# Optimization experiments

Measured on AMD Instinct MI355X. Metric: run time of the kernel, lower is better.

## Reference

```python
import jax, jax.numpy as jnp
import numpy as np

HEADS = 12
EPS = 1e-5

def setup_inputs() -> dict:
    key = jax.random.key(0)
    ks = jax.random.split(key, 24)
    B, T, H = 128, 128, 768
    RIN, RH, NT = 512, 512, 10
    s = 0.02
    inp = {
        'slot_vector': jax.random.normal(ks[0], (B, H), jnp.float32),
        'utt_vectors': jax.random.normal(ks[1], (B, T, H), jnp.float32),
        'Wq': jax.random.normal(ks[2], (H, H), jnp.float32) * s,
        'bq': jnp.zeros((H,), jnp.float32),
        'Wk': jax.random.normal(ks[3], (H, H), jnp.float32) * s,
        'bk': jnp.zeros((H,), jnp.float32),
        'Wv': jax.random.normal(ks[4], (H, H), jnp.float32) * s,
        'bv': jnp.zeros((H,), jnp.float32),
        'Wo': jax.random.normal(ks[5], (H, H), jnp.float32) * s,
        'bo': jnp.zeros((H,), jnp.float32),
        'W_in': jax.random.normal(ks[6], (RIN, 2 * H), jnp.float32) * s,
        'b_in': jnp.zeros((RIN,), jnp.float32),
        'W_ih': jax.random.normal(ks[7], (4 * RH, RIN), jnp.float32) * s,
        'W_hh': jax.random.normal(ks[8], (4 * RH, RH), jnp.float32) * s,
        'b_ih': jnp.zeros((4 * RH,), jnp.float32),
        'b_hh': jnp.zeros((4 * RH,), jnp.float32),
        'W_tag': jax.random.normal(ks[9], (NT, RH), jnp.float32) * s,
        'b_tag': jnp.zeros((NT,), jnp.float32),
        'ln_g': jnp.ones((NT,), jnp.float32),
        'ln_b': jnp.zeros((NT,), jnp.float32),
    }
    return inp

def _forward(slot_vector, utt_vectors, Wq, bq, Wk, bk, Wv, bv, Wo, bo,
             W_in, b_in, W_ih, W_hh, b_ih, b_hh, W_tag, b_tag, ln_g, ln_b):
    B, T, H = utt_vectors.shape
    dk = H // HEADS
    # Multi-head attention: Q is slot vector (seq len 1), K/V are utt encodings
    q = (slot_vector @ Wq.T + bq).reshape(B, 1, HEADS, dk).transpose(0, 2, 1, 3)  # [B,h,1,dk]
    k = (utt_vectors @ Wk.T + bk).reshape(B, T, HEADS, dk).transpose(0, 2, 1, 3)  # [B,h,T,dk]
    v = (utt_vectors @ Wv.T + bv).reshape(B, T, HEADS, dk).transpose(0, 2, 1, 3)
    scores = jnp.einsum('bhqd,bhkd->bhqk', q, k) / jnp.sqrt(jnp.float32(dk))
    attn = jax.nn.softmax(scores, axis=-1)
    X = jnp.einsum('bhqk,bhkd->bhqd', attn, v).transpose(0, 2, 1, 3).reshape(B, H)
    X = X @ Wo.T + bo  # [B, H] context vector, fixed across timesteps
    RH = W_hh.shape[1]
    h0 = jnp.zeros((B, RH), jnp.float32)
    c0 = jnp.zeros((B, RH), jnp.float32)

    def step(carry, x_t):
        h, c = carry
        lstm_in = jax.nn.sigmoid(jnp.concatenate([x_t, X], axis=1) @ W_in.T + b_in)
        gates = lstm_in @ W_ih.T + b_ih + h @ W_hh.T + b_hh  # [B, 4*RH]
        i_g, f_g, g_g, o_g = jnp.split(gates, 4, axis=1)  # torch gate order i,f,g,o
        c = jax.nn.sigmoid(f_g) * c + jax.nn.sigmoid(i_g) * jnp.tanh(g_g)
        h = jax.nn.sigmoid(o_g) * jnp.tanh(c)
        y = h @ W_tag.T + b_tag  # [B, NT]
        mu = jnp.mean(y, axis=-1, keepdims=True)
        var = jnp.mean((y - mu) ** 2, axis=-1, keepdims=True)
        y = (y - mu) / jnp.sqrt(var + EPS) * ln_g + ln_b
        return (h, c), y

    xs = utt_vectors.transpose(1, 0, 2)  # [T, B, H]
    _, ys = jax.lax.scan(step, (h0, c0), xs)  # ys: [T, B, NT]
    return ys.transpose(1, 2, 0)  # [B, NT, T]

def reference(slot_vector, utt_vectors, Wq, bq, Wk, bk, Wv, bv, Wo, bo,
              W_in, b_in, W_ih, W_hh, b_ih, b_hh, W_tag, b_tag, ln_g, ln_b):
    return _forward(slot_vector, utt_vectors, Wq, bq, Wk, bk, Wv, bv, Wo, bo,
                    W_in, b_in, W_ih, W_hh, b_ih, b_hh, W_tag, b_tag, ln_g, ln_b)
```

## Files before the change

kernel.cpp:

```cpp
#include <hip/hip_runtime.h>
#include <hip/hip_bf16.h>
#include <math.h>

#define Bc 128
#define Tc 128
#define Hc 768
#define NHEAD 12
#define DKc 64
#define RHc 512
#define G4c 2048
#define NTc 10
#define LNEPS 1e-5f
#define NSLC 8

typedef short bf16x8 __attribute__((ext_vector_type(8)));
typedef float f32x4 __attribute__((ext_vector_type(4)));

__device__ __forceinline__ float sigmoidf_(float x) { return 1.0f / (1.0f + __expf(-x)); }
__device__ __forceinline__ float tanhf_(float x) { return 1.0f - 2.0f / (__expf(2.0f * x) + 1.0f); }

__device__ __forceinline__ ushort f2bf(float f) {
  union { float f; uint u; } c; c.f = f;
  uint r = (c.u + 0x7FFFu + ((c.u >> 16) & 1u)) >> 16;
  return (ushort)r;
}
__device__ __forceinline__ float bf2f(ushort u) {
  union { uint u; float f; } c; c.u = ((uint)u) << 16;
  return c.f;
}
__device__ __forceinline__ uint pack2(float a, float b) {
  return (uint)f2bf(a) | ((uint)f2bf(b) << 16);
}

__global__ void bias_sum_perm_k(const float* __restrict__ a, const float* __restrict__ b,
                                float* __restrict__ o) {
  int i = blockIdx.x * blockDim.x + threadIdx.x;
  if (i < G4c) {
    const int g = i >> 9, u = i & 511;
    o[u * 4 + g] = a[i] + b[i];
  }
}

__global__ void cvt4_k(const float* __restrict__ x, ushort* __restrict__ y, int n4) {
  int i = blockIdx.x * 256 + threadIdx.x;
  if (i < n4) {
    float4 v = ((const float4*)x)[i];
    ushort4 o; o.x = f2bf(v.x); o.y = f2bf(v.y); o.z = f2bf(v.z); o.w = f2bf(v.w);
    ((ushort4*)y)[i] = o;
  }
}

__global__ __launch_bounds__(256) void cvt_wih_perm_k(
    const float* __restrict__ W, ushort* __restrict__ out)
{
  const int rp = blockIdx.x;
  const int u = rp >> 2, g = rp & 3;
  const float* src = W + (size_t)(g * 512 + u) * 512;
  ushort* dst = out + (size_t)rp * 512;
  for (int k = threadIdx.x; k < 512; k += 256) dst[k] = f2bf(src[k]);
}

__global__ __launch_bounds__(256) void cvt_whh_frag_k(
    const float* __restrict__ Whh, ushort* __restrict__ out)
{
  const int idx = blockIdx.x * 256 + threadIdx.x;
  const int lane = idx & 63;
  const int kf = (idx >> 6) & 15;
  const int ti = idx >> 10;
  const int m = lane & 15;
  const int u = (ti >> 3) * 32 + (ti & 7) * 4 + (m >> 2);
  const int gate = m & 3;
  const int k0 = kf * 32 + (lane >> 4) * 8;
  const float* src = Whh + ((size_t)(gate * RHc + u)) * RHc + k0;
  ushort4 o0, o1;
  o0.x = f2bf(src[0]); o0.y = f2bf(src[1]); o0.z = f2bf(src[2]); o0.w = f2bf(src[3]);
  o1.x = f2bf(src[4]); o1.y = f2bf(src[5]); o1.z = f2bf(src[6]); o1.w = f2bf(src[7]);
  ushort* dst = out + (size_t)idx * 8;
  *(ushort4*)dst = o0;
  *(ushort4*)(dst + 4) = o1;
}

__global__ __launch_bounds__(256) void bgemm_bt(
    const void* __restrict__ Aptr, const ushort* __restrict__ Wb,
    const float* __restrict__ bias, void* __restrict__ Cptr,
    int M, int N, int K, int amode, int outMode,
    const float* __restrict__ utt, const float* __restrict__ xo, int trow0)
{
  __shared__ ushort As[128 * 40];
  __shared__ ushort Ws[128 * 40];
  const int tid = threadIdx.x;
  const int lane = tid & 63, wid = tid >> 6;
  const int wm = wid >> 1, wn = wid & 1;
  const int row0 = blockIdx.y * 128, col0 = blockIdx.x * 128;

  f32x4 acc[4][4];
#pragma unroll
  for (int i = 0; i < 4; ++i)
#pragma unroll
    for (int j = 0; j < 4; ++j) {
      f32x4 z = {0.f, 0.f, 0.f, 0.f};
      acc[i][j] = z;
    }

  const int r = tid >> 1, kq = (tid & 1) * 16;

  for (int kb = 0; kb < K; kb += 32) {
    const int k = kb + kq;
    if (amode == 2) {
      const ushort* ap = (const ushort*)Aptr + (size_t)(row0 + r) * K + k;
      *(uint4*)&As[r * 40 + kq] = *(const uint4*)ap;
      *(uint4*)&As[r * 40 + kq + 8] = *(const uint4*)(ap + 8);
    } else {
      const float* ap;
      if (amode == 0) {
        ap = (const float*)Aptr + (size_t)(row0 + r) * K + k;
      } else {
        const int b = r;
        const int t = trow0 + blockIdx.y;
        ap = (k < Hc) ? utt + ((size_t)b * Tc + t) * Hc + k
                      : xo + (size_t)b * Hc + (k - Hc);
      }
      const float4 f0 = *(const float4*)ap;
      const float4 f1 = *(const float4*)(ap + 4);
      const float4 f2 = *(const float4*)(ap + 8);
      const float4 f3 = *(const float4*)(ap + 12);
      uint4 u0, u1;
      u0.x = pack2(f0.x, f0.y); u0.y = pack2(f0.z, f0.w);
      u0.z = pack2(f1.x, f1.y); u0.w = pack2(f1.z, f1.w);
      u1.x = pack2(f2.x, f2.y); u1.y = pack2(f2.z, f2.w);
      u1.z = pack2(f3.x, f3.y); u1.w = pack2(f3.z, f3.w);
      *(uint4*)&As[r * 40 + kq] = u0;
      *(uint4*)&As[r * 40 + kq + 8] = u1;
    }
    {
      const ushort* wp = Wb + (size_t)(col0 + r) * K + k;
      *(uint4*)&Ws[r * 40 + kq] = *(const uint4*)wp;
      *(uint4*)&Ws[r * 40 + kq + 8] = *(const uint4*)(wp + 8);
    }
    __syncthreads();
    const int koff = (lane >> 4) * 8;
    const int ar = wm * 64 + (lane & 15);
    const int wr = wn * 64 + (lane & 15);
    bf16x8 af[4], wf[4];
#pragma unroll
    for (int i = 0; i < 4; ++i) af[i] = *(const bf16x8*)&As[(ar + i * 16) * 40 + koff];
#pragma unroll
    for (int i = 0; i < 4; ++i) wf[i] = *(const bf16x8*)&Ws[(wr + i * 16) * 40 + koff];
#pragma unroll
    for (int fm = 0; fm < 4; ++fm)
#pragma unroll
      for (int fn = 0; fn < 4; ++fn)
        acc[fm][fn] = __builtin_amdgcn_mfma_f32_16x16x32_bf16(af[fm], wf[fn], acc[fm][fn], 0, 0, 0);
    __syncthreads();
  }

#pragma unroll
  for (int fm = 0; fm < 4; ++fm) {
    const int m0 = row0 + wm * 64 + fm * 16 + ((lane >> 4) * 4);
#pragma unroll
    for (int fn = 0; fn < 4; ++fn) {
      const int n = col0 + wn * 64 + fn * 16 + (lane & 15);
      const float bb = bias[n];
#pragma unroll
      for (int q = 0; q < 4; ++q) {
        const float v = acc[fm][fn][q] + bb;
        if (outMode == 1)
          ((ushort*)Cptr)[(size_t)(m0 + q) * N + n] = f2bf(sigmoidf_(v));
        else
          ((float*)Cptr)[(size_t)(m0 + q) * N + n] = v;
      }
    }
  }
}

__global__ __launch_bounds__(256) void fold_qp_k(
    const float* __restrict__ slot, const float* __restrict__ Wq,
    const float* __restrict__ bq, const float* __restrict__ Wk,
    const float* __restrict__ bk, ushort* __restrict__ Pb, float* __restrict__ cqB)
{
  __shared__ float ss[Hc];
  __shared__ float qp[4][DKc];
  __shared__ float qs[DKc];
  const int bx = blockIdx.x;
  const int b = bx / NHEAD, h = bx % NHEAD;
  const int tid = threadIdx.x;
  for (int i = tid; i < Hc; i += 256) ss[i] = slot[(size_t)b * Hc + i];
  __syncthreads();
  {
    const int d = tid & 63, qt = tid >> 6;
    const float* wr = Wq + (size_t)(h * DKc + d) * Hc + qt * 192;
    const float* sb = ss + qt * 192;
    float a = 0.f;
    for (int e = 0; e < 192; e += 4) {
      const float4 wv = *(const float4*)(wr + e);
      a += wv.x * sb[e] + wv.y * sb[e + 1] + wv.z * sb[e + 2] + wv.w * sb[e + 3];
    }
    qp[qt][d] = a;
  }
  __syncthreads();
  if (tid < DKc)
    qs[tid] = qp[0][tid] + qp[1][tid] + qp[2][tid] + qp[3][tid] + bq[h * DKc + tid];
  __syncthreads();
  if (tid < DKc) {
    float pv = qs[tid] * bk[h * DKc + tid];
#pragma unroll
    for (int off = 32; off; off >>= 1) pv += __shfl_xor(pv, off);
    if (tid == 0) cqB[b * NHEAD + h] = pv;
  }
  for (int j = tid; j < Hc; j += 256) {
    float a = 0.f;
#pragma unroll 8
    for (int d = 0; d < DKc; ++d)
      a = fmaf(qs[d], Wk[(size_t)(h * DKc + d) * Hc + j], a);
    Pb[((size_t)b * NHEAD + h) * Hc + j] = f2bf(a);
  }
}

__global__ __launch_bounds__(256) void attn_scores2_k(
    const ushort* __restrict__ Pb, const float* __restrict__ cqB,
    const float* __restrict__ utt, float* __restrict__ Att)
{
  __shared__ float Phs[NHEAD][Hc];
  __shared__ float sc[NHEAD][Tc];
  const int b = blockIdx.x;
  const int tid = threadIdx.x;
  for (int i = tid; i < NHEAD * Hc; i += 256)
    ((float*)Phs)[i] = bf2f(Pb[(size_t)b * NHEAD * Hc + i]);
  __syncthreads();
  const int t = tid & 127, hh = tid >> 7;
  const int h0 = hh * 6;
  float a6[6];
#pragma unroll
  for (int i = 0; i < 6; ++i) a6[i] = 0.f;
  const float* xr = utt + ((size_t)b * Tc + t) * Hc;
  for (int j = 0; j < Hc; j += 4) {
    const float4 xv = *(const float4*)(xr + j);
#pragma unroll
    for (int i = 0; i < 6; ++i) {
      a6[i] = fmaf(xv.x, Phs[h0 + i][j], a6[i]);
      a6[i] = fmaf(xv.y, Phs[h0 + i][j + 1], a6[i]);
      a6[i] = fmaf(xv.z, Phs[h0 + i][j + 2], a6[i]);
      a6[i] = fmaf(xv.w, Phs[h0 + i][j + 3], a6[i]);
    }
  }
#pragma unroll
  for (int i = 0; i < 6; ++i)
    sc[h0 + i][t] = (a6[i] + cqB[b * NHEAD + h0 + i]) * 0.125f;
  __syncthreads();
  const int w = tid >> 6, lane = tid & 63;
#pragma unroll
  for (int i = 0; i < 3; ++i) {
    const int h = w * 3 + i;
    const float s0 = sc[h][lane], s1 = sc[h][lane + 64];
    float m = fmaxf(s0, s1);
#pragma unroll
    for (int off = 32; off; off >>= 1) m = fmaxf(m, __shfl_xor(m, off));
    const float e0 = expf(s0 - m), e1 = expf(s1 - m);
    float s = e0 + e1;
#pragma unroll
    for (int off = 32; off; off >>= 1) s += __shfl_xor(s, off);
    const float inv = 1.f / s;
    Att[((size_t)b * NHEAD + h) * Tc + lane] = e0 * inv;
    Att[((size_t)b * NHEAD + h) * Tc + lane + 64] = e1 * inv;
  }
}

__global__ __launch_bounds__(256) void attn_uxc_k(
    const float* __restrict__ Att, const float* __restrict__ utt,
    const float* __restrict__ Wv, const float* __restrict__ bv,
    float* __restrict__ Xc)
{
  __shared__ float As[NHEAD][Tc];
  __shared__ float Us[NHEAD * Hc];
  const int b = blockIdx.x;
  const int tid = threadIdx.x;
  for (int i = tid; i < NHEAD * Tc; i += 256)
    ((float*)As)[i] = Att[(size_t)b * NHEAD * Tc + i];
  __syncthreads();
  float acc[NHEAD][3];
#pragma unroll
  for (int h = 0; h < NHEAD; ++h)
#pragma unroll
    for (int q = 0; q < 3; ++q) acc[h][q] = 0.f;
  for (int t = 0; t < Tc; ++t) {
    const float* xr = utt + ((size_t)b * Tc + t) * Hc;
    const float x0 = xr[tid], x1 = xr[tid + 256], x2 = xr[tid + 512];
#pragma unroll
    for (int h = 0; h < NHEAD; ++h) {
      const float a = As[h][t];
      acc[h][0] = fmaf(a, x0, acc[h][0]);
      acc[h][1] = fmaf(a, x1, acc[h][1]);
      acc[h][2] = fmaf(a, x2, acc[h][2]);
    }
  }
#pragma unroll
  for (int h = 0; h < NHEAD; ++h)
#pragma unroll
    for (int q = 0; q < 3; ++q)
      Us[h * Hc + tid + q * 256] = acc[h][q];
  __syncthreads();
#pragma unroll
  for (int rr = 0; rr < 3; ++rr) {
    const int hd = tid + rr * 256;
    const int h = hd >> 6;
    const float* wr = Wv + (size_t)hd * Hc;
    const float* ub = Us + h * Hc;
    float a = 0.f;
    for (int j = 0; j < Hc; j += 4) {
      const float4 w4 = *(const float4*)(wr + j);
      a += w4.x * ub[j] + w4.y * ub[j + 1] + w4.z * ub[j + 2] + w4.w * ub[j + 3];
    }
    Xc[(size_t)b * Hc + hd] = a + bv[hd];
  }
}

__device__ __forceinline__ void group_barrier(unsigned* line) {
  __syncthreads();
  if (threadIdx.x == 0) {
    __builtin_amdgcn_fence(__ATOMIC_RELEASE, "agent");
    unsigned g = __hip_atomic_load(line + 1, __ATOMIC_RELAXED, __HIP_MEMORY_SCOPE_AGENT);
    unsigned a = __hip_atomic_fetch_add(line, 1u, __ATOMIC_ACQ_REL, __HIP_MEMORY_SCOPE_AGENT);
    if (a == NSLC - 1) {
      __hip_atomic_store(line, 0u, __ATOMIC_RELAXED, __HIP_MEMORY_SCOPE_AGENT);
      __hip_atomic_store(line + 1, g + 1u, __ATOMIC_RELEASE, __HIP_MEMORY_SCOPE_AGENT);
    } else {
      while (__hip_atomic_load(line + 1, __ATOMIC_RELAXED, __HIP_MEMORY_SCOPE_AGENT) == g)
        __builtin_amdgcn_s_sleep(1);
      __builtin_amdgcn_fence(__ATOMIC_ACQUIRE, "agent");
    }
  }
  __syncthreads();
}

__global__ __launch_bounds__(512, 1) void lstm_mfma_k(
    const ushort* __restrict__ WhhF, const float* __restrict__ GXc,
    ushort* __restrict__ hbuf, float* __restrict__ Hch,
    float* __restrict__ Cb, int t0, int nsteps, unsigned* __restrict__ bars)
{
  const int blk = blockIdx.x;
  const int gid = blk & 7, sid = blk >> 3;
  const int tid = threadIdx.x;
  const int w = tid >> 6, lane = tid & 63;
  const int bl = lane & 15, uq = lane >> 4;
  const int bglob = gid * 16 + bl;
  unsigned* line = bars + gid * 32;

  const int ti0 = sid * 16 + w * 2;
  const int ug0 = ((ti0 >> 3) << 5) + ((ti0 & 7) << 2) + uq;
  const int ti1 = ti0 + 1;
  const int ug1 = ((ti1 >> 3) << 5) + ((ti1 & 7) << 2) + uq;

  bf16x8 afr0[16], afr1[16];
  {
    const ushort* b0 = WhhF + ((size_t)(ti0 * 16) * 64 + lane) * 8;
    const ushort* b1 = WhhF + ((size_t)(ti1 * 16) * 64 + lane) * 8;
#pragma unroll
    for (int kf = 0; kf < 16; ++kf) {
      afr0[kf] = *(const bf16x8*)(b0 + (size_t)kf * 512);
      afr1[kf] = *(const bf16x8*)(b1 + (size_t)kf * 512);
    }
  }

  float c0 = 0.f, c1 = 0.f;
  if (t0 > 0) {
    c0 = Cb[(size_t)bglob * RHc + ug0];
    c1 = Cb[(size_t)bglob * RHc + ug1];
  }
  ushort* hbg = hbuf + (size_t)gid * (2 * 16 * RHc);

  float4 gxa = *(const float4*)(GXc + ((size_t)0 * Bc + bglob) * G4c + ug0 * 4);
  float4 gxb = *(const float4*)(GXc + ((size_t)0 * Bc + bglob) * G4c + ug1 * 4);

  for (int s = 0; s < nsteps; ++s) {
    const int t = t0 + s;
    f32x4 acc0 = {0.f, 0.f, 0.f, 0.f};
    f32x4 acc1 = {0.f, 0.f, 0.f, 0.f};
    if (t > 0) {
      const ushort* hsrc = hbg + (size_t)((t & 1) ^ 1) * (16 * RHc) + (size_t)bl * RHc + uq * 8;
#pragma unroll
      for (int kf = 0; kf < 16; ++kf) {
        const bf16x8 bf = *(const bf16x8*)(hsrc + kf * 32);
        acc0 = __builtin_amdgcn_mfma_f32_16x16x32_bf16(afr0[kf], bf, acc0, 0, 0, 0);
        acc1 = __builtin_amdgcn_mfma_f32_16x16x32_bf16(afr1[kf], bf, acc1, 0, 0, 0);
      }
    }
    {
      const float iv = sigmoidf_(gxa.x + acc0[0]);
      const float fv = sigmoidf_(gxa.y + acc0[1]);
      const float gv = tanhf_(gxa.z + acc0[2]);
      const float ov = sigmoidf_(gxa.w + acc0[3]);
      c0 = fmaf(fv, c0, iv * gv);
      const float hval = ov * tanhf_(c0);
      hbg[(size_t)(t & 1) * (16 * RHc) + (size_t)bl * RHc + ug0] = f2bf(hval);
      Hch[((size_t)s * Bc + bglob) * RHc + ug0] = hval;
    }
    {
      const float iv = sigmoidf_(gxb.x + acc1[0]);
      const float fv = sigmoidf_(gxb.y + acc1[1]);
      const float gv = tanhf_(gxb.z + acc1[2]);
      const float ov = sigmoidf_(gxb.w + acc1[3]);
      c1 = fmaf(fv, c1, iv * gv);
      const float hval = ov * tanhf_(c1);
      hbg[(size_t)(t & 1) * (16 * RHc) + (size_t)bl * RHc + ug1] = f2bf(hval);
      Hch[((size_t)s * Bc + bglob) * RHc + ug1] = hval;
    }
    if (s != nsteps - 1) {
      gxa = *(const float4*)(GXc + ((size_t)(s + 1) * Bc + bglob) * G4c + ug0 * 4);
      gxb = *(const float4*)(GXc + ((size_t)(s + 1) * Bc + bglob) * G4c + ug1 * 4);
      group_barrier(line);
    }
  }
  Cb[(size_t)bglob * RHc + ug0] = c0;
  Cb[(size_t)bglob * RHc + ug1] = c1;
}

__global__ __launch_bounds__(256) void tag_ln_k(
    const float* __restrict__ Hch, const float* __restrict__ Wtag,
    const float* __restrict__ btag, const float* __restrict__ lng,
    const float* __restrict__ lnb, float* __restrict__ out, int t0)
{
  const int wid = (blockIdx.x * blockDim.x + threadIdx.x) >> 6;
  const int lane = threadIdx.x & 63;
  const int tl = wid >> 7, b = wid & 127;
  const int t = t0 + tl;
  const float* hp = Hch + ((size_t)tl * Bc + b) * RHc;
  float y[NTc];
#pragma unroll
  for (int j = 0; j < NTc; ++j) y[j] = 0.f;
  for (int k = lane; k < RHc; k += 64) {
    const float hv = hp[k];
#pragma unroll
    for (int j = 0; j < NTc; ++j)
      y[j] = fmaf(hv, Wtag[(size_t)j * RHc + k], y[j]);
  }
#pragma unroll
  for (int off = 32; off > 0; off >>= 1)
#pragma unroll
    for (int j = 0; j < NTc; ++j)
      y[j] += __shfl_xor(y[j], off);
  float mu = 0.f;
#pragma unroll
  for (int j = 0; j < NTc; ++j) { y[j] += btag[j]; mu += y[j]; }
  mu *= (1.0f / NTc);
  float var = 0.f;
#pragma unroll
  for (int j = 0; j < NTc; ++j) { const float d = y[j] - mu; var = fmaf(d, d, var); }
  var *= (1.0f / NTc);
  const float inv = rsqrtf(var + LNEPS);
  if (lane < NTc) {
    out[(size_t)b * NTc * Tc + (size_t)lane * Tc + t] =
        (y[lane] - mu) * inv * lng[lane] + lnb[lane];
  }
}

extern "C" void kernel_launch(void* const* d_in, const int* in_sizes, int n_in,
                              void* d_out, int out_size, void* d_ws, size_t ws_size,
                              hipStream_t stream)
{
  const float* slot = (const float*)d_in[0];
  const float* utt  = (const float*)d_in[1];
  const float* Wq = (const float*)d_in[2];   const float* bq = (const float*)d_in[3];
  const float* Wk = (const float*)d_in[4];   const float* bk = (const float*)d_in[5];
  const float* Wv = (const float*)d_in[6];   const float* bv = (const float*)d_in[7];
  const float* Wo = (const float*)d_in[8];   const float* bo = (const float*)d_in[9];
  const float* W_in = (const float*)d_in[10]; const float* b_in = (const float*)d_in[11];
  const float* W_ih = (const float*)d_in[12]; const float* W_hh = (const float*)d_in[13];
  const float* b_ih = (const float*)d_in[14]; const float* b_hh = (const float*)d_in[15];
  const float* W_tag = (const float*)d_in[16]; const float* b_tag = (const float*)d_in[17];
  const float* ln_g = (const float*)d_in[18]; const float* ln_b = (const float*)d_in[19];
  float* out = (float*)d_out;
  float* ws = (float*)d_ws;

  int CHT = 16;
  while (CHT > 2 && 4ull * (2265088ull + 360448ull * (unsigned)CHT) > ws_size)
    CHT >>= 1;
  const int NCH = Tc / CHT;

  float* Xc    = ws;
  float* Xo    = Xc + 98304;
  float* bsum  = Xo + 98304;
  float* Cb    = bsum + 2048;
  float* Att   = Cb + 65536;
  ushort* hbuf = (ushort*)(Att + 196608);
  ushort* WinB = (ushort*)(ws + 526336);
  ushort* WihB = (ushort*)(ws + 919552);
  ushort* WoB  = (ushort*)(ws + 1443840);
  ushort* WhhF = (ushort*)(ws + 1738752);
  float* cqB   = ws + 2263040;
  unsigned* bars = (unsigned*)(ws + 2264576);
  ushort* LINc = (ushort*)(ws + 2265088);
  float* GXc   = ws + 2265088 + (size_t)32768 * CHT;
  float* Hch   = GXc + (size_t)262144 * CHT;
  ushort* Pb   = (ushort*)(ws + 2265088);

  (void)hipMemsetAsync(bars, 0, 2048, stream);

  hipLaunchKernelGGL(cvt4_k, dim3(768), dim3(256), 0, stream, W_in, WinB, 196608);
  hipLaunchKernelGGL(cvt_wih_perm_k, dim3(2048), dim3(256), 0, stream, W_ih, WihB);
  hipLaunchKernelGGL(cvt4_k, dim3(576), dim3(256), 0, stream, Wo, WoB, 147456);
  hipLaunchKernelGGL(cvt_whh_frag_k, dim3(512), dim3(256), 0, stream, W_hh, WhhF);
  hipLaunchKernelGGL(bias_sum_perm_k, dim3(8), dim3(256), 0, stream, b_ih, b_hh, bsum);

  hipLaunchKernelGGL(fold_qp_k, dim3(Bc * NHEAD), dim3(256), 0, stream,
                     slot, Wq, bq, Wk, bk, Pb, cqB);
  hipLaunchKernelGGL(attn_scores2_k, dim3(Bc), dim3(256), 0, stream, Pb, cqB, utt, Att);
  hipLaunchKernelGGL(attn_uxc_k, dim3(Bc), dim3(256), 0, stream, Att, utt, Wv, bv, Xc);
  hipLaunchKernelGGL(bgemm_bt, dim3(6, 1), dim3(256), 0, stream,
                     (const void*)Xc, WoB, bo, (void*)Xo, 128, 768, 768, 0, 0,
                     (const float*)nullptr, (const float*)nullptr, 0);

  for (int tc = 0; tc < NCH; ++tc) {
    hipLaunchKernelGGL(bgemm_bt, dim3(4, CHT), dim3(256), 0, stream,
                       (const void*)nullptr, WinB, b_in, (void*)LINc,
                       CHT * Bc, 512, 1536, 1, 1, utt, Xo, tc * CHT);
    hipLaunchKernelGGL(bgemm_bt, dim3(16, CHT), dim3(256), 0, stream,
                       (const void*)LINc, WihB, bsum, (void*)GXc,
                       CHT * Bc, 2048, 512, 2, 0,
                       (const float*)nullptr, (const float*)nullptr, 0);
    hipLaunchKernelGGL(lstm_mfma_k, dim3(64), dim3(512), 0, stream,
                       WhhF, GXc, hbuf, Hch, Cb, tc * CHT, CHT, bars);
    hipLaunchKernelGGL(tag_ln_k, dim3(CHT * 32), dim3(256), 0, stream,
                       Hch, W_tag, b_tag, ln_g, ln_b, out, tc * CHT);
  }
}
```

Measured before the change: 2.134 ms.

## Replace counter-based group barrier with per-slice step flags in LSTM kernel

Swaps the atomic fetch-add group barrier between the 8 cooperating blocks for per-slice monotonic flags. Each block publishes its completed step with a release store and then waits on the peers' flags only before the next recurrent matmul. This drops the serialized fetch-add and the generation reset, and lets a block overlap its gate-input prefetch with the wait. The h exchange now uses agent-scope atomic loads and stores to keep it coherent. Flags are never reset, so the bars buffer must be zeroed per launch, which looks fragile across the t0 chunks.

```diff
diff --git a/kernel.cpp b/kernel.cpp
--- a/kernel.cpp
+++ b/kernel.cpp
@@ -314,24 +314,6 @@
   }
 }
 
-__device__ __forceinline__ void group_barrier(unsigned* line) {
-  __syncthreads();
-  if (threadIdx.x == 0) {
-    __builtin_amdgcn_fence(__ATOMIC_RELEASE, "agent");
-    unsigned g = __hip_atomic_load(line + 1, __ATOMIC_RELAXED, __HIP_MEMORY_SCOPE_AGENT);
-    unsigned a = __hip_atomic_fetch_add(line, 1u, __ATOMIC_ACQ_REL, __HIP_MEMORY_SCOPE_AGENT);
-    if (a == NSLC - 1) {
-      __hip_atomic_store(line, 0u, __ATOMIC_RELAXED, __HIP_MEMORY_SCOPE_AGENT);
-      __hip_atomic_store(line + 1, g + 1u, __ATOMIC_RELEASE, __HIP_MEMORY_SCOPE_AGENT);
-    } else {
-      while (__hip_atomic_load(line + 1, __ATOMIC_RELAXED, __HIP_MEMORY_SCOPE_AGENT) == g)
-        __builtin_amdgcn_s_sleep(1);
-      __builtin_amdgcn_fence(__ATOMIC_ACQUIRE, "agent");
-    }
-  }
-  __syncthreads();
-}
-
 __global__ __launch_bounds__(512, 1) void lstm_mfma_k(
     const ushort* __restrict__ WhhF, const float* __restrict__ GXc,
     ushort* __restrict__ hbuf, float* __restrict__ Hch,
@@ -343,7 +325,7 @@
   const int w = tid >> 6, lane = tid & 63;
   const int bl = lane & 15, uq = lane >> 4;
   const int bglob = gid * 16 + bl;
-  unsigned* line = bars + gid * 32;
+  unsigned* flags = bars + gid * 16;
 
   const int ti0 = sid * 16 + w * 2;
   const int ug0 = ((ti0 >> 3) << 5) + ((ti0 & 7) << 2) + uq;
@@ -376,14 +358,26 @@
     f32x4 acc0 = {0.f, 0.f, 0.f, 0.f};
     f32x4 acc1 = {0.f, 0.f, 0.f, 0.f};
     if (t > 0) {
+      if (s > 0) {
+        if (tid < NSLC) {
+          while (__hip_atomic_load(&flags[tid], __ATOMIC_ACQUIRE,
+                                   __HIP_MEMORY_SCOPE_AGENT) < (unsigned)t)
+            __builtin_amdgcn_s_sleep(2);
+        }
+        __syncthreads();
+      }
       const ushort* hsrc = hbg + (size_t)((t & 1) ^ 1) * (16 * RHc) + (size_t)bl * RHc + uq * 8;
 #pragma unroll
       for (int kf = 0; kf < 16; ++kf) {
-        const bf16x8 bf = *(const bf16x8*)(hsrc + kf * 32);
-        acc0 = __builtin_amdgcn_mfma_f32_16x16x32_bf16(afr0[kf], bf, acc0, 0, 0, 0);
-        acc1 = __builtin_amdgcn_mfma_f32_16x16x32_bf16(afr1[kf], bf, acc1, 0, 0, 0);
+        union { bf16x8 v; unsigned long long q[2]; } hu;
+        const unsigned long long* hp = (const unsigned long long*)(hsrc + kf * 32);
+        hu.q[0] = __hip_atomic_load(hp, __ATOMIC_RELAXED, __HIP_MEMORY_SCOPE_AGENT);
+        hu.q[1] = __hip_atomic_load(hp + 1, __ATOMIC_RELAXED, __HIP_MEMORY_SCOPE_AGENT);
+        acc0 = __builtin_amdgcn_mfma_f32_16x16x32_bf16(afr0[kf], hu.v, acc0, 0, 0, 0);
+        acc1 = __builtin_amdgcn_mfma_f32_16x16x32_bf16(afr1[kf], hu.v, acc1, 0, 0, 0);
       }
     }
+    ushort* hdst = hbg + (size_t)(t & 1) * (16 * RHc) + (size_t)bl * RHc;
     {
       const float iv = sigmoidf_(gxa.x + acc0[0]);
       const float fv = sigmoidf_(gxa.y + acc0[1]);
@@ -391,7 +385,7 @@
       const float ov = sigmoidf_(gxa.w + acc0[3]);
       c0 = fmaf(fv, c0, iv * gv);
       const float hval = ov * tanhf_(c0);
-      hbg[(size_t)(t & 1) * (16 * RHc) + (size_t)bl * RHc + ug0] = f2bf(hval);
+      __hip_atomic_store(&hdst[ug0], f2bf(hval), __ATOMIC_RELAXED, __HIP_MEMORY_SCOPE_AGENT);
       Hch[((size_t)s * Bc + bglob) * RHc + ug0] = hval;
     }
     {
@@ -401,13 +395,16 @@
       const float ov = sigmoidf_(gxb.w + acc1[3]);
       c1 = fmaf(fv, c1, iv * gv);
       const float hval = ov * tanhf_(c1);
-      hbg[(size_t)(t & 1) * (16 * RHc) + (size_t)bl * RHc + ug1] = f2bf(hval);
+      __hip_atomic_store(&hdst[ug1], f2bf(hval), __ATOMIC_RELAXED, __HIP_MEMORY_SCOPE_AGENT);
       Hch[((size_t)s * Bc + bglob) * RHc + ug1] = hval;
     }
     if (s != nsteps - 1) {
       gxa = *(const float4*)(GXc + ((size_t)(s + 1) * Bc + bglob) * G4c + ug0 * 4);
       gxb = *(const float4*)(GXc + ((size_t)(s + 1) * Bc + bglob) * G4c + ug1 * 4);
-      group_barrier(line);
+      __syncthreads();
+      if (tid == 0)
+        __hip_atomic_store(&flags[sid], (unsigned)(t + 1), __ATOMIC_RELEASE,
+                           __HIP_MEMORY_SCOPE_AGENT);
     }
   }
   Cb[(size_t)bglob * RHc + ug0] = c0;
```

Result: slower. 2.368 ms (+10.9%).
